# Kernel tuning notes

Hardware: AMD Instinct MI355X
Metric: run time of the kernel (lower is better)

## Reference

```python
import jax, jax.numpy as jnp
import numpy as np
import math

EMBED_DIM = 1024
WINDOW = 512


def setup_inputs() -> dict:
    key = jax.random.key(0)
    k_x, k_mb, k_wg, k_bg = jax.random.split(key, 4)
    x = jax.random.normal(k_x, (4, 4096, EMBED_DIM), dtype=jnp.float32)
    memory_bank = jax.random.normal(k_mb, (WINDOW, EMBED_DIM), dtype=jnp.float32)
    # memory_gate: nn.Linear(embed_dim, embed_dim)
    lim = 1.0 / math.sqrt(EMBED_DIM)
    gate_w = jax.random.uniform(k_wg, (EMBED_DIM, EMBED_DIM), jnp.float32, -lim, lim)
    gate_b = jax.random.uniform(k_bg, (EMBED_DIM,), jnp.float32, -lim, lim)
    return {"x": x, "memory_bank": memory_bank, "gate_w": gate_w, "gate_b": gate_b}


def reference(x, memory_bank, gate_w, gate_b):
    d = x.shape[-1]
    # attention scores over fixed memory bank: [B, S, W]
    scores = jnp.einsum("bsd,wd->bsw", x, memory_bank) / jnp.sqrt(jnp.asarray(d, x.dtype))
    attn = jax.nn.softmax(scores, axis=-1)
    retrieved = jnp.einsum("bsw,wd->bsd", attn, memory_bank)
    gate = jax.nn.sigmoid(jnp.einsum("bsd,ed->bse", x, gate_w) + gate_b)
    return gate * x + (1.0 - gate) * retrieved
```

## Files before the change

kernel.cpp:

```cpp
#include <hip/hip_runtime.h>
#include <hip/hip_bf16.h>

#define EMBED 1024
#define WINDOW 512
#define NROWS 16384

typedef __attribute__((ext_vector_type(4))) float f32x4;
typedef __bf16 bf16x8 __attribute__((ext_vector_type(8)));

#define GLDS(g, l)                                                        \
  __builtin_amdgcn_global_load_lds(                                       \
      (const __attribute__((address_space(1))) void*)(const void*)(g),    \
      (__attribute__((address_space(3))) void*)(void*)(l), 16, 0, 0)

__global__ __launch_bounds__(256) void cast_bf16_kernel(
    const float* __restrict__ in, __bf16* __restrict__ out, int n8) {
  int i = blockIdx.x * blockDim.x + threadIdx.x;
  if (i >= n8) return;
  const f32x4* p = (const f32x4*)(in + (size_t)i * 8);
  f32x4 a = p[0], b = p[1];
  bf16x8 o = {(__bf16)a[0], (__bf16)a[1], (__bf16)a[2], (__bf16)a[3],
              (__bf16)b[0], (__bf16)b[1], (__bf16)b[2], (__bf16)b[3]};
  *(bf16x8*)(out + (size_t)i * 8) = o;
}

__global__ __launch_bounds__(256) void transpose_mb_lds_kernel(
    const float* __restrict__ mb, __bf16* __restrict__ mbt) {
  __shared__ __bf16 tile[32][33];
  const int tx = threadIdx.x & 7, ty = threadIdx.x >> 3;
  const int w0 = (blockIdx.x & 15) * 32;
  const int d0 = (blockIdx.x >> 4) * 32;
  f32x4 v = *(const f32x4*)(mb + (size_t)(w0 + ty) * EMBED + d0 + tx * 4);
#pragma unroll
  for (int j = 0; j < 4; ++j) tile[tx * 4 + j][ty] = (__bf16)v[j];
  __syncthreads();
  unsigned u0 =
      ((unsigned)__builtin_bit_cast(unsigned short, tile[ty][tx * 4 + 1]) << 16) |
      (unsigned)__builtin_bit_cast(unsigned short, tile[ty][tx * 4 + 0]);
  unsigned u1 =
      ((unsigned)__builtin_bit_cast(unsigned short, tile[ty][tx * 4 + 3]) << 16) |
      (unsigned)__builtin_bit_cast(unsigned short, tile[ty][tx * 4 + 2]);
  uint2 w2 = {u0, u1};
  *(uint2*)(mbt + (size_t)(d0 + ty) * WINDOW + w0 + tx * 4) = w2;
}

__global__ __launch_bounds__(512, 1) void scores_mega_kernel(
    const float* __restrict__ x, const __bf16* __restrict__ mbb,
    __bf16* __restrict__ xb, __bf16* __restrict__ s1) {
  __shared__ __align__(16) __bf16 ldsA[3][64 * 32];
  __shared__ __align__(16) __bf16 ldsB[3][512 * 32];
  __shared__ float sred[8][64];
  __shared__ float sfin[64];
  const int tid = threadIdx.x, lane = tid & 63, wave = tid >> 6;
  const int row0 = blockIdx.x * 64;
  const int warp_n = wave;
  const int fr = lane & 15, fq = lane >> 4;

  const int arow = tid >> 3;
  const int ag = (tid >> 1) & 3;
  const int ah = tid & 1;
  const int fA = (arow & 3) ^ ((arow >> 2) & 3);
  const int aws = arow * 32 + ((ag ^ fA) * 8) + ah * 4;
  const float* aSrc = x + (size_t)(row0 + arow) * EMBED + (tid & 7) * 4;
  __bf16* xbDst = xb + (size_t)(row0 + arow) * EMBED + (tid & 7) * 4;

  const int srow = lane >> 2;
  const int sgc = (lane & 3) ^ ((lane >> 2) & 3) ^ ((lane >> 4) & 3);
  const __bf16* bSrc = mbb + (size_t)(wave * 64 + srow) * EMBED + sgc * 8;

#define STG_B(t, buf)                                                         \
  {                                                                           \
    _Pragma("unroll") for (int c = 0; c < 4; ++c)                             \
        GLDS(bSrc + (size_t)c * 16 * EMBED + (t) * 32,                        \
             &ldsB[buf][(wave * 64 + c * 16) * 32]);                          \
  }

#define PACK_WRITE(av, buf, t)                                                \
  {                                                                           \
    unsigned u0 =                                                             \
        ((unsigned)__builtin_bit_cast(unsigned short, (__bf16)av[1]) << 16) | \
        (unsigned)__builtin_bit_cast(unsigned short, (__bf16)av[0]);          \
    unsigned u1 =                                                             \
        ((unsigned)__builtin_bit_cast(unsigned short, (__bf16)av[3]) << 16) | \
        (unsigned)__builtin_bit_cast(unsigned short, (__bf16)av[2]);          \
    uint2 w2 = {u0, u1};                                                      \
    *(uint2*)(&ldsA[buf][aws]) = w2;                                          \
    *(uint2*)(xbDst + (t) * 32) = w2;                                         \
  }

#define MCOMPUTE(cur)                                                         \
  {                                                                           \
    const __bf16* As_ = &ldsA[cur][0];                                        \
    const __bf16* Bs_ = &ldsB[cur][(warp_n * 64) * 32];                       \
    const int pg_ = (fq ^ ((fr & 3) ^ ((fr >> 2) & 3))) * 8;                  \
    bf16x8 af[4], bfv[4];                                                     \
    _Pragma("unroll") for (int m = 0; m < 4; ++m)                             \
        af[m] = *(const bf16x8*)(As_ + (m * 16 + fr) * 32 + pg_);             \
    _Pragma("unroll") for (int n = 0; n < 4; ++n)                             \
        bfv[n] = *(const bf16x8*)(Bs_ + (n * 16 + fr) * 32 + pg_);            \
    asm volatile("s_waitcnt lgkmcnt(0)" ::: "memory");                        \
    __builtin_amdgcn_s_setprio(1);                                            \
    _Pragma("unroll") for (int m = 0; m < 4; ++m)                             \
        _Pragma("unroll") for (int n = 0; n < 4; ++n)                         \
            acc[m][n] = __builtin_amdgcn_mfma_f32_16x16x32_bf16(              \
                af[m], bfv[n], acc[m][n], 0, 0, 0);                           \
    __builtin_amdgcn_s_setprio(0);                                            \
  }

#define TBODY(t, APACK, ALOAD)                                                \
  {                                                                           \
    if ((t) + 2 < 32) {                                                       \
      ALOAD = *(const f32x4*)(aSrc + ((t) + 2) * 32);                         \
      asm volatile("" ::: "memory");                                          \
      STG_B((t) + 2, rs2);                                                    \
    }                                                                         \
    MCOMPUTE(rs0);                                                            \
    if ((t) + 1 < 32) {                                                       \
      if ((t) + 2 < 32) {                                                     \
        asm volatile("s_waitcnt vmcnt(10)" ::: "memory");                     \
      } else {                                                                \
        asm volatile("s_waitcnt vmcnt(5)" ::: "memory");                      \
      }                                                                       \
      PACK_WRITE(APACK, rs1, (t) + 1);                                        \
      if ((t) + 2 < 32) {                                                     \
        asm volatile("s_waitcnt vmcnt(7)" ::: "memory");                      \
      } else {                                                                \
        asm volatile("s_waitcnt vmcnt(2)" ::: "memory");                      \
      }                                                                       \
      asm volatile("s_waitcnt lgkmcnt(0)" ::: "memory");                      \
    }                                                                         \
    __builtin_amdgcn_s_barrier();                                             \
    const int tmp_ = rs0; rs0 = rs1; rs1 = rs2; rs2 = tmp_;                   \
  }

  f32x4 acc[4][4];
#pragma unroll
  for (int m = 0; m < 4; ++m)
#pragma unroll
    for (int n = 0; n < 4; ++n) acc[m][n] = (f32x4){0.f, 0.f, 0.f, 0.f};

  int rs0 = 0, rs1 = 1, rs2 = 2;
  f32x4 aE, aO;
  {
    f32x4 a0 = *(const f32x4*)(aSrc);
    asm volatile("" ::: "memory");
    STG_B(0, 0);
    aO = *(const f32x4*)(aSrc + 32);
    asm volatile("" ::: "memory");
    STG_B(1, 1);
    asm volatile("s_waitcnt vmcnt(9)" ::: "memory");
    PACK_WRITE(a0, 0, 0);
    asm volatile("s_waitcnt lgkmcnt(0)" ::: "memory");
    __builtin_amdgcn_s_barrier();
  }

  for (int t = 0; t < 32; t += 2) {
    TBODY(t, aO, aE);
    TBODY(t + 1, aE, aO);
  }
#undef TBODY
#undef STG_B
#undef PACK_WRITE
#undef MCOMPUTE

  const float scale = 0.03125f;
  float rmx[4][4];
#pragma unroll
  for (int m = 0; m < 4; ++m)
#pragma unroll
    for (int j = 0; j < 4; ++j) {
      float v = -1e30f;
#pragma unroll
      for (int n = 0; n < 4; ++n) {
        acc[m][n][j] *= scale;
        v = fmaxf(v, acc[m][n][j]);
      }
      rmx[m][j] = v;
    }
#pragma unroll
  for (int off = 1; off < 16; off <<= 1)
#pragma unroll
    for (int m = 0; m < 4; ++m)
#pragma unroll
      for (int j = 0; j < 4; ++j)
        rmx[m][j] = fmaxf(rmx[m][j], __shfl_xor(rmx[m][j], off));
  if (fr == 0) {
#pragma unroll
    for (int m = 0; m < 4; ++m)
#pragma unroll
      for (int j = 0; j < 4; ++j) sred[warp_n][m * 16 + fq * 4 + j] = rmx[m][j];
  }
  __syncthreads();
  if (tid < 64) {
    float v = sred[0][tid];
#pragma unroll
    for (int w = 1; w < 8; ++w) v = fmaxf(v, sred[w][tid]);
    sfin[tid] = v;
  }
  __syncthreads();

  float rsm[4][4];
#pragma unroll
  for (int m = 0; m < 4; ++m)
#pragma unroll
    for (int j = 0; j < 4; ++j) {
      const float fm = sfin[m * 16 + fq * 4 + j];
      float s = 0.f;
#pragma unroll
      for (int n = 0; n < 4; ++n) {
        float e = __expf(acc[m][n][j] - fm);
        acc[m][n][j] = e;
        s += e;
      }
      rsm[m][j] = s;
    }
#pragma unroll
  for (int off = 1; off < 16; off <<= 1)
#pragma unroll
    for (int m = 0; m < 4; ++m)
#pragma unroll
      for (int j = 0; j < 4; ++j) rsm[m][j] += __shfl_xor(rsm[m][j], off);
  if (fr == 0) {
#pragma unroll
    for (int m = 0; m < 4; ++m)
#pragma unroll
      for (int j = 0; j < 4; ++j) sred[warp_n][m * 16 + fq * 4 + j] = rsm[m][j];
  }
  __syncthreads();
  if (tid < 64) {
    float v = sred[0][tid];
#pragma unroll
    for (int w = 1; w < 8; ++w) v += sred[w][tid];
    sfin[tid] = 1.0f / v;
  }
  __syncthreads();

#pragma unroll
  for (int m = 0; m < 4; ++m)
#pragma unroll
    for (int j = 0; j < 4; ++j) {
      const int row = row0 + m * 16 + fq * 4 + j;
      const float inv = sfin[m * 16 + fq * 4 + j];
#pragma unroll
      for (int n = 0; n < 4; ++n)
        s1[(size_t)row * WINDOW + warp_n * 64 + n * 16 + fr] =
            (__bf16)(acc[m][n][j] * inv);
    }
}

__global__ __launch_bounds__(256, 2) void dual_fused128_kernel(
    const __bf16* __restrict__ s1, const __bf16* __restrict__ xb,
    const __bf16* __restrict__ mbt, const __bf16* __restrict__ gwb,
    const float* __restrict__ gb, float* __restrict__ out) {
  __shared__ __align__(16) __bf16 ldsA[2][128 * 64];
  __shared__ __align__(16) __bf16 ldsB[2][128 * 64];
  const int tid = threadIdx.x, lane = tid & 63, wave = tid >> 6;
  const int bid = blockIdx.x;
  const int xcd = bid & 7;
  const int g = bid >> 3;
  const int bm = xcd * 16 + (g >> 3);
  const int bn = g & 7;
  const int row0 = bm * 128, col0 = bn * 128;
  const int warp_m = wave >> 1, warp_n = wave & 1;
  const int fr = lane & 15, fq = lane >> 4;
  const int srow = lane >> 3;
  const int sgc = (lane & 7) ^ srow;
  const int wv32 = wave * 32;

  const __bf16* aR = s1 + (size_t)(row0 + wv32 + srow) * WINDOW + sgc * 8;
  const __bf16* bR = mbt + (size_t)(col0 + wv32 + srow) * WINDOW + sgc * 8;
  const __bf16* aG = xb + (size_t)(row0 + wv32 + srow) * EMBED + sgc * 8;
  const __bf16* bG = gwb + (size_t)(col0 + wv32 + srow) * EMBED + sgc * 8;

#define STG(vt, buf)                                                          \
  {                                                                           \
    if ((vt) < 8) {                                                           \
      const int k0_ = (vt)*64;                                                \
      _Pragma("unroll") for (int c = 0; c < 4; ++c)                           \
          GLDS(aR + (size_t)c * 8 * WINDOW + k0_,                             \
               &ldsA[buf][(wv32 + c * 8) * 64]);                              \
      _Pragma("unroll") for (int c = 0; c < 4; ++c)                           \
          GLDS(bR + (size_t)c * 8 * WINDOW + k0_,                             \
               &ldsB[buf][(wv32 + c * 8) * 64]);                              \
    } else {                                                                  \
      const int k0_ = ((vt)-8) * 64;                                          \
      _Pragma("unroll") for (int c = 0; c < 4; ++c)                           \
          GLDS(aG + (size_t)c * 8 * EMBED + k0_,                              \
               &ldsA[buf][(wv32 + c * 8) * 64]);                              \
      _Pragma("unroll") for (int c = 0; c < 4; ++c)                           \
          GLDS(bG + (size_t)c * 8 * EMBED + k0_,                              \
               &ldsB[buf][(wv32 + c * 8) * 64]);                              \
    }                                                                         \
  }

#define BARF                                                                  \
  {                                                                           \
    asm volatile("" ::: "memory");                                            \
    __builtin_amdgcn_s_barrier();                                             \
    asm volatile("" ::: "memory");                                            \
  }

#define COMPUTE(ACC, cur)                                                     \
  {                                                                           \
    const __bf16* As_ = &ldsA[cur][(warp_m * 64 + fr) * 64];                  \
    const __bf16* Bs_ = &ldsB[cur][(warp_n * 64 + fr) * 64];                  \
    _Pragma("unroll") for (int kk = 0; kk < 2; ++kk) {                        \
      const int pg_ = ((kk * 4 + fq) ^ (fr & 7)) * 8;                         \
      bf16x8 af[4], bfv[4];                                                   \
      _Pragma("unroll") for (int m = 0; m < 4; ++m)                           \
          af[m] = *(const bf16x8*)(As_ + m * 16 * 64 + pg_);                  \
      _Pragma("unroll") for (int n = 0; n < 4; ++n)                           \
          bfv[n] = *(const bf16x8*)(Bs_ + n * 16 * 64 + pg_);                 \
      __builtin_amdgcn_s_setprio(1);                                          \
      _Pragma("unroll") for (int m = 0; m < 4; ++m)                           \
          _Pragma("unroll") for (int n = 0; n < 4; ++n)                       \
              ACC[m][n] = __builtin_amdgcn_mfma_f32_16x16x32_bf16(            \
                  af[m], bfv[n], ACC[m][n], 0, 0, 0);                         \
      __builtin_amdgcn_s_setprio(0);                                          \
    }                                                                         \
  }

  f32x4 accr[4][4], accg[4][4];
#pragma unroll
  for (int m = 0; m < 4; ++m)
#pragma unroll
    for (int n = 0; n < 4; ++n) {
      accr[m][n] = (f32x4){0.f, 0.f, 0.f, 0.f};
      accg[m][n] = (f32x4){0.f, 0.f, 0.f, 0.f};
    }

  STG(0, 0);
  for (int vt = 0; vt < 8; ++vt) {
    const int cur = vt & 1;
    STG(vt + 1, cur ^ 1);
    asm volatile("s_waitcnt vmcnt(8)" ::: "memory");
    BARF;
    COMPUTE(accr, cur);
    BARF;
  }
  for (int vt = 8; vt < 24; ++vt) {
    const int cur = vt & 1;
    if (vt + 1 < 24) {
      STG(vt + 1, cur ^ 1);
      asm volatile("s_waitcnt vmcnt(8)" ::: "memory");
    } else {
      asm volatile("s_waitcnt vmcnt(0)" ::: "memory");
    }
    BARF;
    COMPUTE(accg, cur);
    BARF;
  }
#undef STG
#undef COMPUTE
#undef BARF

#pragma unroll
  for (int n = 0; n < 4; ++n) {
    const int col = col0 + warp_n * 64 + n * 16 + fr;
    const float bias = gb[col];
#pragma unroll
    for (int m = 0; m < 4; ++m) {
#pragma unroll
      for (int j = 0; j < 4; ++j) {
        const int row = row0 + warp_m * 64 + m * 16 + fq * 4 + j;
        const size_t o = (size_t)row * EMBED + col;
        const float gt = 1.0f / (1.0f + __expf(-(accg[m][n][j] + bias)));
        const float xv = (float)xb[o];
        out[o] = gt * xv + (1.0f - gt) * accr[m][n][j];
      }
    }
  }
}

extern "C" void kernel_launch(void* const* d_in, const int* in_sizes, int n_in,
                              void* d_out, int out_size, void* d_ws,
                              size_t ws_size, hipStream_t stream) {
  const float* x = (const float*)d_in[0];
  const float* mb = (const float*)d_in[1];
  const float* gw = (const float*)d_in[2];
  const float* gb = (const float*)d_in[3];
  float* out = (float*)d_out;

  char* ws = (char*)d_ws;
  __bf16* xb = (__bf16*)(ws);
  __bf16* mbb = (__bf16*)(ws + 33554432);
  __bf16* mbt = (__bf16*)(ws + 34603008);
  __bf16* gwb = (__bf16*)(ws + 35651584);
  __bf16* s1 = (__bf16*)(ws + 37748736);

  cast_bf16_kernel<<<256, 256, 0, stream>>>(mb, mbb, 65536);
  cast_bf16_kernel<<<512, 256, 0, stream>>>(gw, gwb, 131072);
  transpose_mb_lds_kernel<<<512, 256, 0, stream>>>(mb, mbt);
  scores_mega_kernel<<<256, 512, 0, stream>>>(x, mbb, xb, s1);
  dual_fused128_kernel<<<1024, 256, 0, stream>>>(s1, xb, mbt, gwb, gb, out);
}
```

Before: 122.9 us.

## Load B operands directly from global into registers, skipping LDS staging

```diff
diff --git a/kernel.cpp b/kernel.cpp
--- a/kernel.cpp
+++ b/kernel.cpp
@@ -48,7 +48,6 @@
     const float* __restrict__ x, const __bf16* __restrict__ mbb,
     __bf16* __restrict__ xb, __bf16* __restrict__ s1) {
   __shared__ __align__(16) __bf16 ldsA[3][64 * 32];
-  __shared__ __align__(16) __bf16 ldsB[3][512 * 32];
   __shared__ float sred[8][64];
   __shared__ float sfin[64];
   const int tid = threadIdx.x, lane = tid & 63, wave = tid >> 6;
@@ -64,16 +63,7 @@
   const float* aSrc = x + (size_t)(row0 + arow) * EMBED + (tid & 7) * 4;
   __bf16* xbDst = xb + (size_t)(row0 + arow) * EMBED + (tid & 7) * 4;
 
-  const int srow = lane >> 2;
-  const int sgc = (lane & 3) ^ ((lane >> 2) & 3) ^ ((lane >> 4) & 3);
-  const __bf16* bSrc = mbb + (size_t)(wave * 64 + srow) * EMBED + sgc * 8;
-
-#define STG_B(t, buf)                                                         \
-  {                                                                           \
-    _Pragma("unroll") for (int c = 0; c < 4; ++c)                             \
-        GLDS(bSrc + (size_t)c * 16 * EMBED + (t) * 32,                        \
-             &ldsB[buf][(wave * 64 + c * 16) * 32]);                          \
-  }
+  const __bf16* bP = mbb + (size_t)(warp_n * 64 + fr) * EMBED + fq * 8;
 
 #define PACK_WRITE(av, buf, t)                                                \
   {                                                                           \
@@ -88,17 +78,15 @@
     *(uint2*)(xbDst + (t) * 32) = w2;                                         \
   }
 
-#define MCOMPUTE(cur)                                                         \
+#define MCOMPUTE(cur, t)                                                      \
   {                                                                           \
     const __bf16* As_ = &ldsA[cur][0];                                        \
-    const __bf16* Bs_ = &ldsB[cur][(warp_n * 64) * 32];                       \
     const int pg_ = (fq ^ ((fr & 3) ^ ((fr >> 2) & 3))) * 8;                  \
     bf16x8 af[4], bfv[4];                                                     \
+    _Pragma("unroll") for (int n = 0; n < 4; ++n)                             \
+        bfv[n] = *(const bf16x8*)(bP + (size_t)(n * 16) * EMBED + (t) * 32);  \
     _Pragma("unroll") for (int m = 0; m < 4; ++m)                             \
         af[m] = *(const bf16x8*)(As_ + (m * 16 + fr) * 32 + pg_);             \
-    _Pragma("unroll") for (int n = 0; n < 4; ++n)                             \
-        bfv[n] = *(const bf16x8*)(Bs_ + (n * 16 + fr) * 32 + pg_);            \
-    asm volatile("s_waitcnt lgkmcnt(0)" ::: "memory");                        \
     __builtin_amdgcn_s_setprio(1);                                            \
     _Pragma("unroll") for (int m = 0; m < 4; ++m)                             \
         _Pragma("unroll") for (int n = 0; n < 4; ++n)                         \
@@ -109,26 +97,10 @@
 
 #define TBODY(t, APACK, ALOAD)                                                \
   {                                                                           \
-    if ((t) + 2 < 32) {                                                       \
-      ALOAD = *(const f32x4*)(aSrc + ((t) + 2) * 32);                         \
-      asm volatile("" ::: "memory");                                          \
-      STG_B((t) + 2, rs2);                                                    \
-    }                                                                         \
-    MCOMPUTE(rs0);                                                            \
-    if ((t) + 1 < 32) {                                                       \
-      if ((t) + 2 < 32) {                                                     \
-        asm volatile("s_waitcnt vmcnt(10)" ::: "memory");                     \
-      } else {                                                                \
-        asm volatile("s_waitcnt vmcnt(5)" ::: "memory");                      \
-      }                                                                       \
-      PACK_WRITE(APACK, rs1, (t) + 1);                                        \
-      if ((t) + 2 < 32) {                                                     \
-        asm volatile("s_waitcnt vmcnt(7)" ::: "memory");                      \
-      } else {                                                                \
-        asm volatile("s_waitcnt vmcnt(2)" ::: "memory");                      \
-      }                                                                       \
-      asm volatile("s_waitcnt lgkmcnt(0)" ::: "memory");                      \
-    }                                                                         \
+    if ((t) + 2 < 32) ALOAD = *(const f32x4*)(aSrc + ((t) + 2) * 32);         \
+    MCOMPUTE(rs0, t);                                                         \
+    if ((t) + 1 < 32) PACK_WRITE(APACK, rs1, (t) + 1);                        \
+    asm volatile("s_waitcnt lgkmcnt(0)" ::: "memory");                        \
     __builtin_amdgcn_s_barrier();                                             \
     const int tmp_ = rs0; rs0 = rs1; rs1 = rs2; rs2 = tmp_;                   \
   }
@@ -143,12 +115,7 @@
   f32x4 aE, aO;
   {
     f32x4 a0 = *(const f32x4*)(aSrc);
-    asm volatile("" ::: "memory");
-    STG_B(0, 0);
     aO = *(const f32x4*)(aSrc + 32);
-    asm volatile("" ::: "memory");
-    STG_B(1, 1);
-    asm volatile("s_waitcnt vmcnt(9)" ::: "memory");
     PACK_WRITE(a0, 0, 0);
     asm volatile("s_waitcnt lgkmcnt(0)" ::: "memory");
     __builtin_amdgcn_s_barrier();
@@ -159,7 +126,6 @@
     TBODY(t + 1, aE, aO);
   }
 #undef TBODY
-#undef STG_B
 #undef PACK_WRITE
 #undef MCOMPUTE
 
@@ -248,12 +214,11 @@
     }
 }
 
-__global__ __launch_bounds__(256, 2) void dual_fused128_kernel(
+__global__ __launch_bounds__(256) void dual_bdir_kernel(
     const __bf16* __restrict__ s1, const __bf16* __restrict__ xb,
     const __bf16* __restrict__ mbt, const __bf16* __restrict__ gwb,
     const float* __restrict__ gb, float* __restrict__ out) {
-  __shared__ __align__(16) __bf16 ldsA[2][128 * 64];
-  __shared__ __align__(16) __bf16 ldsB[2][128 * 64];
+  __shared__ __align__(16) __bf16 ldsA[3][128 * 64];
   const int tid = threadIdx.x, lane = tid & 63, wave = tid >> 6;
   const int bid = blockIdx.x;
   const int xcd = bid & 7;
@@ -268,56 +233,58 @@
   const int wv32 = wave * 32;
 
   const __bf16* aR = s1 + (size_t)(row0 + wv32 + srow) * WINDOW + sgc * 8;
-  const __bf16* bR = mbt + (size_t)(col0 + wv32 + srow) * WINDOW + sgc * 8;
   const __bf16* aG = xb + (size_t)(row0 + wv32 + srow) * EMBED + sgc * 8;
-  const __bf16* bG = gwb + (size_t)(col0 + wv32 + srow) * EMBED + sgc * 8;
-
-#define STG(vt, buf)                                                          \
+  const __bf16* bRp = mbt + (size_t)(col0 + warp_n * 64 + fr) * WINDOW + fq * 8;
+  const __bf16* bGp = gwb + (size_t)(col0 + warp_n * 64 + fr) * EMBED + fq * 8;
+
+#define STG_A(vt, slot)                                                       \
   {                                                                           \
     if ((vt) < 8) {                                                           \
       const int k0_ = (vt)*64;                                                \
       _Pragma("unroll") for (int c = 0; c < 4; ++c)                           \
           GLDS(aR + (size_t)c * 8 * WINDOW + k0_,                             \
-               &ldsA[buf][(wv32 + c * 8) * 64]);                              \
-      _Pragma("unroll") for (int c = 0; c < 4; ++c)                           \
-          GLDS(bR + (size_t)c * 8 * WINDOW + k0_,                             \
-               &ldsB[buf][(wv32 + c * 8) * 64]);                              \
+               &ldsA[slot][(wv32 + c * 8) * 64]);                             \
     } else {                                                                  \
       const int k0_ = ((vt)-8) * 64;                                          \
       _Pragma("unroll") for (int c = 0; c < 4; ++c)                           \
           GLDS(aG + (size_t)c * 8 * EMBED + k0_,                              \
-               &ldsA[buf][(wv32 + c * 8) * 64]);                              \
-      _Pragma("unroll") for (int c = 0; c < 4; ++c)                           \
-          GLDS(bG + (size_t)c * 8 * EMBED + k0_,                              \
-               &ldsB[buf][(wv32 + c * 8) * 64]);                              \
+               &ldsA[slot][(wv32 + c * 8) * 64]);                             \
     }                                                                         \
   }
 
-#define BARF                                                                  \
-  {                                                                           \
-    asm volatile("" ::: "memory");                                            \
+#define DTILE(ACC, vt, BP, LDB_, KB)                                          \
+  {                                                                           \
+    if ((vt) < 23) {                                                          \
+      asm volatile("s_waitcnt vmcnt(4)" ::: "memory");                        \
+    } else {                                                                  \
+      asm volatile("s_waitcnt vmcnt(0)" ::: "memory");                        \
+    }                                                                         \
     __builtin_amdgcn_s_barrier();                                             \
-    asm volatile("" ::: "memory");                                            \
-  }
-
-#define COMPUTE(ACC, cur)                                                     \
-  {                                                                           \
-    const __bf16* As_ = &ldsA[cur][(warp_m * 64 + fr) * 64];                  \
-    const __bf16* Bs_ = &ldsB[cur][(warp_n * 64 + fr) * 64];                  \
-    _Pragma("unroll") for (int kk = 0; kk < 2; ++kk) {                        \
-      const int pg_ = ((kk * 4 + fq) ^ (fr & 7)) * 8;                         \
-      bf16x8 af[4], bfv[4];                                                   \
-      _Pragma("unroll") for (int m = 0; m < 4; ++m)                           \
-          af[m] = *(const bf16x8*)(As_ + m * 16 * 64 + pg_);                  \
-      _Pragma("unroll") for (int n = 0; n < 4; ++n)                           \
-          bfv[n] = *(const bf16x8*)(Bs_ + n * 16 * 64 + pg_);                 \
-      __builtin_amdgcn_s_setprio(1);                                          \
-      _Pragma("unroll") for (int m = 0; m < 4; ++m)                           \
-          _Pragma("unroll") for (int n = 0; n < 4; ++n)                       \
-              ACC[m][n] = __builtin_amdgcn_mfma_f32_16x16x32_bf16(            \
-                  af[m], bfv[n], ACC[m][n], 0, 0, 0);                         \
-      __builtin_amdgcn_s_setprio(0);                                          \
+    bf16x8 b0[4], b1[4];                                                      \
+    _Pragma("unroll") for (int n = 0; n < 4; ++n) {                           \
+      b0[n] = *(const bf16x8*)(BP + (size_t)(n * 16) * LDB_ + (KB));          \
+      b1[n] = *(const bf16x8*)(BP + (size_t)(n * 16) * LDB_ + (KB) + 32);     \
     }                                                                         \
+    if ((vt) + 2 < 24) STG_A((vt) + 2, ((vt) + 2) % 3);                       \
+    const __bf16* As_ = &ldsA[(vt) % 3][(warp_m * 64 + fr) * 64];             \
+    bf16x8 af[4];                                                             \
+    _Pragma("unroll") for (int m = 0; m < 4; ++m)                             \
+        af[m] = *(const bf16x8*)(As_ + m * 16 * 64 + ((fq ^ (fr & 7)) * 8));  \
+    __builtin_amdgcn_s_setprio(1);                                            \
+    _Pragma("unroll") for (int m = 0; m < 4; ++m)                             \
+        _Pragma("unroll") for (int n = 0; n < 4; ++n)                         \
+            ACC[m][n] = __builtin_amdgcn_mfma_f32_16x16x32_bf16(              \
+                af[m], b0[n], ACC[m][n], 0, 0, 0);                            \
+    __builtin_amdgcn_s_setprio(0);                                            \
+    _Pragma("unroll") for (int m = 0; m < 4; ++m)                             \
+        af[m] = *(const bf16x8*)(As_ + m * 16 * 64 +                          \
+                                 (((4 + fq) ^ (fr & 7)) * 8));                \
+    __builtin_amdgcn_s_setprio(1);                                            \
+    _Pragma("unroll") for (int m = 0; m < 4; ++m)                             \
+        _Pragma("unroll") for (int n = 0; n < 4; ++n)                         \
+            ACC[m][n] = __builtin_amdgcn_mfma_f32_16x16x32_bf16(              \
+                af[m], b1[n], ACC[m][n], 0, 0, 0);                            \
+    __builtin_amdgcn_s_setprio(0);                                            \
   }
 
   f32x4 accr[4][4], accg[4][4];
@@ -329,30 +296,17 @@
       accg[m][n] = (f32x4){0.f, 0.f, 0.f, 0.f};
     }
 
-  STG(0, 0);
+  STG_A(0, 0);
+  STG_A(1, 1);
+
   for (int vt = 0; vt < 8; ++vt) {
-    const int cur = vt & 1;
-    STG(vt + 1, cur ^ 1);
-    asm volatile("s_waitcnt vmcnt(8)" ::: "memory");
-    BARF;
-    COMPUTE(accr, cur);
-    BARF;
+    DTILE(accr, vt, bRp, WINDOW, vt * 64);
   }
   for (int vt = 8; vt < 24; ++vt) {
-    const int cur = vt & 1;
-    if (vt + 1 < 24) {
-      STG(vt + 1, cur ^ 1);
-      asm volatile("s_waitcnt vmcnt(8)" ::: "memory");
-    } else {
-      asm volatile("s_waitcnt vmcnt(0)" ::: "memory");
-    }
-    BARF;
-    COMPUTE(accg, cur);
-    BARF;
-  }
-#undef STG
-#undef COMPUTE
-#undef BARF
+    DTILE(accg, vt, bGp, EMBED, (vt - 8) * 64);
+  }
+#undef DTILE
+#undef STG_A
 
 #pragma unroll
   for (int n = 0; n < 4; ++n) {
@@ -392,5 +346,5 @@
   cast_bf16_kernel<<<512, 256, 0, stream>>>(gw, gwb, 131072);
   transpose_mb_lds_kernel<<<512, 256, 0, stream>>>(mb, mbt);
   scores_mega_kernel<<<256, 512, 0, stream>>>(x, mbb, xb, s1);
-  dual_fused128_kernel<<<1024, 256, 0, stream>>>(s1, xb, mbt, gwb, gb, out);
-}
+  dual_bdir_kernel<<<1024, 256, 0, stream>>>(s1, xb, mbt, gwb, gb, out);
+}
```

Result: slower. 183.4 us (+49.2%).
